# Performance work log

Measured on AMD Instinct MI355X. Metric: run time of the kernel, lower is better.

Reference implementation:

```python
import jax, jax.numpy as jnp
import numpy as np

EPS = 1e-6  # torch F.pairwise_distance default eps (added to the elementwise difference)
XI = 1.2


def _pdist(A, B):
    # dist[i, j] = || B[j] - A[i] + EPS ||_2  == || (B[j]+EPS) - A[i] ||_2
    Bp = B + EPS
    sq = (jnp.sum(Bp * Bp, axis=-1)[None, :]
          + jnp.sum(A * A, axis=-1)[:, None]
          - 2.0 * A @ Bp.T)
    return jnp.sqrt(jnp.maximum(sq, 0.0))


def _half_loss(D, M):
    # D: [B, B] distances, row i = anchor. M: [B, B] float same-label mask.
    same_max = jnp.max(D * M, axis=1)                      # max over same-label distances
    diff = D * (1.0 - M)                                   # zero at same-label slots
    diff_max = jnp.max(diff, axis=1)
    # replace same-label slots with diff_max so min picks the smallest diff-label distance
    diff_min = jnp.min(M * diff_max[:, None] + diff, axis=1)
    l = same_max - diff_min + XI
    return jnp.sum(jax.nn.relu(l))


def setup_inputs() -> dict:
    key = jax.random.key(0)
    k1, k2, k3 = jax.random.split(key, 3)
    B, d = 4096, 1024
    v_f = jax.random.normal(k1, (B, d), dtype=jnp.float32)
    i_f = jax.random.normal(k2, (B, d), dtype=jnp.float32)
    y = jax.random.randint(k3, (B,), 0, 64, dtype=jnp.int64)
    return {"v_f": v_f, "i_f": i_f, "y": y}


def reference(v_f, i_f, y):
    M = (y[:, None] == y[None, :]).astype(v_f.dtype)
    # loop 1: anchor i_f[i] vs all v_f  -> D1[i, j] = ||v_f[j] - i_f[i] + eps||
    loss_i = _half_loss(_pdist(i_f, v_f), M)
    # loop 2: anchor v_f[i] vs all i_f  -> D2[i, j] = ||i_f[j] - v_f[i] + eps||
    loss_v = _half_loss(_pdist(v_f, i_f), M)
    return loss_i + loss_v
```

## Files before the change

kernel.cpp:

```cpp
#include <hip/hip_runtime.h>
#include <hip/hip_bf16.h>


#define MDIM 4096
#define KDIM 1024
#define NT   16

typedef __attribute__((ext_vector_type(4))) float  f32x4;
typedef __attribute__((ext_vector_type(8))) short  bf16x8;

__device__ __forceinline__ void gload16(const void* g, void* l) {
  __builtin_amdgcn_global_load_lds(
      (const __attribute__((address_space(1))) void*)g,
      (__attribute__((address_space(3))) void*)l,
      16, 0, 0);
}

__device__ __forceinline__ unsigned short f2bf(float x) {
  unsigned int u = __float_as_uint(x);
  unsigned int r = (u + 0x7FFFu + ((u >> 16) & 1u)) >> 16;
  return (unsigned short)r;
}

#define BAR() do { asm volatile("" ::: "memory"); \
                   __builtin_amdgcn_s_barrier();  \
                   asm volatile("" ::: "memory"); } while (0)

__global__ __launch_bounds__(256) void prep_kernel(
    const float* __restrict__ vf, const float* __restrict__ iff,
    unsigned short* __restrict__ vb, unsigned short* __restrict__ ib,
    float* __restrict__ ni, float* __restrict__ nvp,
    int* __restrict__ same_sq, int* __restrict__ diff_sq,
    float* __restrict__ out) {
  const int wid = blockIdx.x * 4 + (threadIdx.x >> 6);
  const int lane = threadIdx.x & 63;
  const int mat = wid >> 12;
  const int row = wid & 4095;
  const float* X = mat ? iff : vf;
  unsigned short* Xb = mat ? ib : vb;

  const float4* xr4 = (const float4*)(X + (size_t)row * KDIM);
  ushort4* xb4 = (ushort4*)(Xb + (size_t)row * KDIM);

  float4 v = xr4[lane];
  ushort4 o;
  o.x = f2bf(v.x); o.y = f2bf(v.y); o.z = f2bf(v.z); o.w = f2bf(v.w);
  xb4[lane] = o;

  float s;
  if (mat) {
    s = v.x * v.x + v.y * v.y + v.z * v.z + v.w * v.w;
  } else {
    float ex = v.x + 1e-6f, ey = v.y + 1e-6f, ez = v.z + 1e-6f, ew = v.w + 1e-6f;
    s = ex * ex + ey * ey + ez * ez + ew * ew;
  }
  for (int off = 32; off; off >>= 1) s += __shfl_down(s, off);
  if (lane == 0) {
    if (mat) ni[row] = s; else nvp[row] = s;
  }

  const int gi = blockIdx.x * 256 + threadIdx.x;
  if (gi < 2 * MDIM) {
    same_sq[gi] = 0;
    diff_sq[gi] = 0x7F800000;
  }
  if (gi == 0) out[0] = 0.0f;
}

__global__ __launch_bounds__(512, 2) void tri_gemm(
    const unsigned short* __restrict__ vb, const unsigned short* __restrict__ ib,
    const float* __restrict__ ni, const float* __restrict__ nvp,
    const int* __restrict__ y,
    int* __restrict__ same_sq, int* __restrict__ diff_sq) {
  __shared__ unsigned short Abuf[2][256][64];
  __shared__ unsigned short Bbuf[2][256][64];
  __shared__ int   yrow[256], ycol[256];
  __shared__ float nAr[256], nBc[256];

  const unsigned short* Amat = ib;
  const unsigned short* Bmat = vb;

  const int row0 = blockIdx.y * 256;
  const int col0 = blockIdx.x * 256;

  const int t = threadIdx.x;
  const int w = t >> 6, lane = t & 63;
  const int lr = lane & 15, lg = lane >> 4;
  const int wr = w >> 2, wc = w & 3;

  auto stage = [&](const unsigned short* __restrict__ X, int tile0,
                   unsigned short (&buf)[256][64], int h, int k0s) {
#pragma unroll
    for (int r = 0; r < 2; ++r) {
      const int row = h * 128 + r * 64 + (t >> 3);
      const int chunk = t & 7;
      const unsigned short* src =
          X + (size_t)(tile0 + row) * KDIM + k0s + ((chunk ^ (row & 7)) << 3);
      gload16(src, &buf[h * 128 + r * 64 + (w << 3)][0]);
    }
  };
  auto ldA = [&](int c, int mh, int m, int ks) -> bf16x8 {
    const int row = wr * 128 + mh * 64 + m * 16 + lr;
    const int chunk = ((ks << 2) | lg) ^ (row & 7);
    return *(const bf16x8*)&Abuf[c][row][chunk << 3];
  };
  auto ldB = [&](int c, int nh, int n, int ks) -> bf16x8 {
    const int col = wc * 64 + nh * 32 + n * 16 + lr;
    const int chunk = ((ks << 2) | lg) ^ (col & 7);
    return *(const bf16x8*)&Bbuf[c][col][chunk << 3];
  };

  stage(Amat, row0, Abuf[0], 0, 0);
  stage(Amat, row0, Abuf[0], 1, 0);
  stage(Bmat, col0, Bbuf[0], 0, 0);
  stage(Bmat, col0, Bbuf[0], 1, 0);
  stage(Amat, row0, Abuf[1], 0, 64);
  if (t < 256) {
    yrow[t] = y[row0 + t];
    nAr[t] = ni[row0 + t];
  } else {
    const int c = t - 256;
    ycol[c] = y[col0 + c];
    nBc[c] = nvp[col0 + c];
  }
  asm volatile("s_waitcnt vmcnt(4) lgkmcnt(0)" ::: "memory");
  BAR();

  f32x4 acc[8][4] = {};
  bf16x8 aF[4][2], bF0[2][2], bF1[2][2];

#define DO_TILE(C, K1, K2)                                                     \
  do {                                                                         \
                              \
    _Pragma("unroll") for (int m = 0; m < 4; ++m) {                            \
      aF[m][0] = ldA(C, 0, m, 0);                                              \
      aF[m][1] = ldA(C, 0, m, 1);                                              \
    }                                                                          \
    _Pragma("unroll") for (int n = 0; n < 2; ++n) {                            \
      bF0[n][0] = ldB(C, 0, n, 0);                                             \
      bF0[n][1] = ldB(C, 0, n, 1);                                             \
    }                                                                          \
    stage(Amat, row0, Abuf[1 - (C)], 1, (K1));                                 \
    asm volatile("s_waitcnt lgkmcnt(8)" ::: "memory");                         \
    BAR();                                                                     \
    __builtin_amdgcn_s_setprio(1);                                             \
    _Pragma("unroll") for (int m = 0; m < 4; ++m)                              \
      _Pragma("unroll") for (int n = 0; n < 2; ++n) {                          \
        acc[m][n] = __builtin_amdgcn_mfma_f32_16x16x32_bf16(                   \
            aF[m][0], bF0[n][0], acc[m][n], 0, 0, 0);                          \
        acc[m][n] = __builtin_amdgcn_mfma_f32_16x16x32_bf16(                   \
            aF[m][1], bF0[n][1], acc[m][n], 0, 0, 0);                          \
      }                                                                        \
    __builtin_amdgcn_s_setprio(0);                                             \
    asm volatile("s_waitcnt vmcnt(4)" ::: "memory");                           \
    BAR();                                                                     \
                              \
    _Pragma("unroll") for (int n = 0; n < 2; ++n) {                            \
      bF1[n][0] = ldB(C, 1, n, 0);                                             \
      bF1[n][1] = ldB(C, 1, n, 1);                                             \
    }                                                                          \
    stage(Bmat, col0, Bbuf[1 - (C)], 0, (K1));                                 \
    BAR();                                                                     \
    __builtin_amdgcn_s_setprio(1);                                             \
    _Pragma("unroll") for (int m = 0; m < 4; ++m)                              \
      _Pragma("unroll") for (int n = 0; n < 2; ++n) {                          \
        acc[m][2 + n] = __builtin_amdgcn_mfma_f32_16x16x32_bf16(               \
            aF[m][0], bF1[n][0], acc[m][2 + n], 0, 0, 0);                      \
        acc[m][2 + n] = __builtin_amdgcn_mfma_f32_16x16x32_bf16(               \
            aF[m][1], bF1[n][1], acc[m][2 + n], 0, 0, 0);                      \
      }                                                                        \
    __builtin_amdgcn_s_setprio(0);                                             \
    BAR();                                                                     \
                              \
    _Pragma("unroll") for (int m = 0; m < 4; ++m) {                            \
      aF[m][0] = ldA(C, 1, m, 0);                                              \
      aF[m][1] = ldA(C, 1, m, 1);                                              \
    }                                                                          \
    stage(Bmat, col0, Bbuf[1 - (C)], 1, (K1));                                 \
    BAR();                                                                     \
    __builtin_amdgcn_s_setprio(1);                                             \
    _Pragma("unroll") for (int m = 0; m < 4; ++m)                              \
      _Pragma("unroll") for (int n = 0; n < 2; ++n) {                          \
        acc[4 + m][n] = __builtin_amdgcn_mfma_f32_16x16x32_bf16(               \
            aF[m][0], bF0[n][0], acc[4 + m][n], 0, 0, 0);                      \
        acc[4 + m][n] = __builtin_amdgcn_mfma_f32_16x16x32_bf16(               \
            aF[m][1], bF0[n][1], acc[4 + m][n], 0, 0, 0);                      \
      }                                                                        \
    __builtin_amdgcn_s_setprio(0);                                             \
    BAR();                                                                     \
                   \
    stage(Amat, row0, Abuf[C], 0, (K2));                                       \
    BAR();                                                                     \
    __builtin_amdgcn_s_setprio(1);                                             \
    _Pragma("unroll") for (int m = 0; m < 4; ++m)                              \
      _Pragma("unroll") for (int n = 0; n < 2; ++n) {                          \
        acc[4 + m][2 + n] = __builtin_amdgcn_mfma_f32_16x16x32_bf16(           \
            aF[m][0], bF1[n][0], acc[4 + m][2 + n], 0, 0, 0);                  \
        acc[4 + m][2 + n] = __builtin_amdgcn_mfma_f32_16x16x32_bf16(           \
            aF[m][1], bF1[n][1], acc[4 + m][2 + n], 0, 0, 0);                  \
      }                                                                        \
    __builtin_amdgcn_s_setprio(0);                                             \
    asm volatile("s_waitcnt vmcnt(4)" ::: "memory");                           \
    BAR();                                                                     \
  } while (0)

  for (int kt = 0; kt < NT; kt += 2) {
    const int ka = ((kt + 1) & (NT - 1)) * 64;
    const int kb = ((kt + 2) & (NT - 1)) * 64;
    const int kc = ((kt + 3) & (NT - 1)) * 64;
    DO_TILE(0, ka, kb);
    DO_TILE(1, kb, kc);
  }
#undef DO_TILE
  asm volatile("s_waitcnt vmcnt(0)" ::: "memory");

  const int rbase0 = row0;
  const int rbase1 = MDIM + col0;
  const float INF = __int_as_float(0x7F800000);

  float cs[4], cd[4];
#pragma unroll
  for (int N = 0; N < 4; ++N) { cs[N] = 0.0f; cd[N] = INF; }

#pragma unroll
  for (int M = 0; M < 8; ++M) {
#pragma unroll
    for (int r = 0; r < 4; ++r) {
      const int row_loc = wr * 128 + M * 16 + lg * 4 + r;
      const float na = nAr[row_loc];
      const int yl = yrow[row_loc];
      float smax = 0.0f;
      float dmin = INF;
#pragma unroll
      for (int N = 0; N < 4; ++N) {
        const int col_loc = wc * 64 + N * 16 + lr;
        const float sq = fmaxf(na + nBc[col_loc] - 2.0f * acc[M][N][r], 0.0f);
        if (ycol[col_loc] == yl) {
          smax = fmaxf(smax, sq);
          cs[N] = fmaxf(cs[N], sq);
        } else {
          dmin = fminf(dmin, sq);
          cd[N] = fminf(cd[N], sq);
        }
      }
#pragma unroll
      for (int off = 1; off < 16; off <<= 1) {
        smax = fmaxf(smax, __shfl_xor(smax, off));
        dmin = fminf(dmin, __shfl_xor(dmin, off));
      }
      if (lr == 0) {
        atomicMax(&same_sq[rbase0 + row_loc], __float_as_int(smax));
        atomicMin(&diff_sq[rbase0 + row_loc], __float_as_int(dmin));
      }
    }
  }
#pragma unroll
  for (int N = 0; N < 4; ++N) {
    float s = cs[N], d = cd[N];
    s = fmaxf(s, __shfl_xor(s, 16)); d = fminf(d, __shfl_xor(d, 16));
    s = fmaxf(s, __shfl_xor(s, 32)); d = fminf(d, __shfl_xor(d, 32));
    if (lane < 16) {
      const int col_loc = wc * 64 + N * 16 + lr;
      atomicMax(&same_sq[rbase1 + col_loc], __float_as_int(s));
      atomicMin(&diff_sq[rbase1 + col_loc], __float_as_int(d));
    }
  }
}

__global__ __launch_bounds__(256) void finalize_kernel(
    const int* __restrict__ same_sq, const int* __restrict__ diff_sq,
    float* __restrict__ out) {
  const int i = blockIdx.x * 256 + threadIdx.x;
  const float sm = sqrtf(__int_as_float(same_sq[i]));
  const float dm = sqrtf(__int_as_float(diff_sq[i]));
  float l = fmaxf(sm - dm + 1.2f, 0.0f);
  for (int off = 32; off; off >>= 1) l += __shfl_down(l, off);
  __shared__ float part[4];
  const int w = threadIdx.x >> 6, lane = threadIdx.x & 63;
  if (lane == 0) part[w] = l;
  __syncthreads();
  if (threadIdx.x == 0) atomicAdd(out, part[0] + part[1] + part[2] + part[3]);
}

extern "C" void kernel_launch(void* const* d_in, const int* in_sizes, int n_in,
                              void* d_out, int out_size, void* d_ws, size_t ws_size,
                              hipStream_t stream) {
  const float* vf = (const float*)d_in[0];
  const float* iff = (const float*)d_in[1];
  const int* y = (const int*)d_in[2];
  float* out = (float*)d_out;

  char* ws = (char*)d_ws;
  unsigned short* vb = (unsigned short*)ws;
  unsigned short* ib = (unsigned short*)(ws + (8u << 20));
  float* nv  = (float*)(ws + (16u << 20));
  float* ni  = nv + 4096;
  float* nvp = nv + 2 * 4096;
  int* same_sq = (int*)(nv + 4 * 4096);
  int* diff_sq = same_sq + 2 * 4096;

  prep_kernel<<<2048, 256, 0, stream>>>(vf, iff, vb, ib, ni, nvp,
                                        same_sq, diff_sq, out);
  tri_gemm<<<dim3(16, 16), 512, 0, stream>>>(vb, ib, ni, nvp, y,
                                             same_sq, diff_sq);
  finalize_kernel<<<32, 256, 0, stream>>>(same_sq, diff_sq, out);
}
```

Baseline: 55.91 us.

## Use 1024-thread blocks with 16 waves each owning a 64x64 sub-tile

Doubles the workgroup from 8 to 16 waves over the same 256x256 output tile. Each wave now accumulates a 64x64 region instead of 128x64, which halves accumulator registers. Each thread issues one global-to-LDS load per stage instead of two, and the prologue waitcnt and per-tile waitcnt are adjusted to match. This aims to add latency hiding through more resident waves, at the cost of more barrier participants and lower MFMA work per LDS fragment load.

New measurement: 65.04 us. +16.3%, slower.

```diff
diff --git a/kernel.cpp b/kernel.cpp
--- a/kernel.cpp
+++ b/kernel.cpp
@@ -67,7 +67,7 @@
   if (gi == 0) out[0] = 0.0f;
 }
 
-__global__ __launch_bounds__(512, 2) void tri_gemm(
+__global__ __launch_bounds__(1024, 4) void tri_gemm(
     const unsigned short* __restrict__ vb, const unsigned short* __restrict__ ib,
     const float* __restrict__ ni, const float* __restrict__ nvp,
     const int* __restrict__ y,
@@ -90,17 +90,14 @@
 
   auto stage = [&](const unsigned short* __restrict__ X, int tile0,
                    unsigned short (&buf)[256][64], int h, int k0s) {
-#pragma unroll
-    for (int r = 0; r < 2; ++r) {
-      const int row = h * 128 + r * 64 + (t >> 3);
-      const int chunk = t & 7;
-      const unsigned short* src =
-          X + (size_t)(tile0 + row) * KDIM + k0s + ((chunk ^ (row & 7)) << 3);
-      gload16(src, &buf[h * 128 + r * 64 + (w << 3)][0]);
-    }
+    const int row = h * 128 + (t >> 3);
+    const int chunk = t & 7;
+    const unsigned short* src =
+        X + (size_t)(tile0 + row) * KDIM + k0s + ((chunk ^ (row & 7)) << 3);
+    gload16(src, &buf[h * 128 + (w << 3)][0]);
   };
   auto ldA = [&](int c, int mh, int m, int ks) -> bf16x8 {
-    const int row = wr * 128 + mh * 64 + m * 16 + lr;
+    const int row = wr * 64 + mh * 32 + m * 16 + lr;
     const int chunk = ((ks << 2) | lg) ^ (row & 7);
     return *(const bf16x8*)&Abuf[c][row][chunk << 3];
   };
@@ -115,92 +112,80 @@
   stage(Bmat, col0, Bbuf[0], 0, 0);
   stage(Bmat, col0, Bbuf[0], 1, 0);
   stage(Amat, row0, Abuf[1], 0, 64);
+  stage(Amat, row0, Abuf[1], 1, 64);
   if (t < 256) {
     yrow[t] = y[row0 + t];
     nAr[t] = ni[row0 + t];
-  } else {
+  } else if (t < 512) {
     const int c = t - 256;
     ycol[c] = y[col0 + c];
     nBc[c] = nvp[col0 + c];
   }
-  asm volatile("s_waitcnt vmcnt(4) lgkmcnt(0)" ::: "memory");
+  asm volatile("s_waitcnt vmcnt(2) lgkmcnt(0)" ::: "memory");
   BAR();
 
-  f32x4 acc[8][4] = {};
-  bf16x8 aF[4][2], bF0[2][2], bF1[2][2];
+  f32x4 acc[4][4] = {};
+  bf16x8 aF[2][2], bF0[2][2], bF1[2][2];
 
 #define DO_TILE(C, K1, K2)                                                     \
   do {                                                                         \
-                              \
-    _Pragma("unroll") for (int m = 0; m < 4; ++m) {                            \
-      aF[m][0] = ldA(C, 0, m, 0);                                              \
-      aF[m][1] = ldA(C, 0, m, 1);                                              \
-    }                                                                          \
-    _Pragma("unroll") for (int n = 0; n < 2; ++n) {                            \
-      bF0[n][0] = ldB(C, 0, n, 0);                                             \
-      bF0[n][1] = ldB(C, 0, n, 1);                                             \
-    }                                                                          \
-    stage(Amat, row0, Abuf[1 - (C)], 1, (K1));                                 \
-    asm volatile("s_waitcnt lgkmcnt(8)" ::: "memory");                         \
-    BAR();                                                                     \
-    __builtin_amdgcn_s_setprio(1);                                             \
-    _Pragma("unroll") for (int m = 0; m < 4; ++m)                              \
-      _Pragma("unroll") for (int n = 0; n < 2; ++n) {                          \
-        acc[m][n] = __builtin_amdgcn_mfma_f32_16x16x32_bf16(                   \
-            aF[m][0], bF0[n][0], acc[m][n], 0, 0, 0);                          \
-        acc[m][n] = __builtin_amdgcn_mfma_f32_16x16x32_bf16(                   \
-            aF[m][1], bF0[n][1], acc[m][n], 0, 0, 0);                          \
-      }                                                                        \
-    __builtin_amdgcn_s_setprio(0);                                             \
-    asm volatile("s_waitcnt vmcnt(4)" ::: "memory");                           \
-    BAR();                                                                     \
-                              \
-    _Pragma("unroll") for (int n = 0; n < 2; ++n) {                            \
-      bF1[n][0] = ldB(C, 1, n, 0);                                             \
-      bF1[n][1] = ldB(C, 1, n, 1);                                             \
-    }                                                                          \
+                      \
+    _Pragma("unroll") for (int m = 0; m < 2; ++m)                              \
+      _Pragma("unroll") for (int ks = 0; ks < 2; ++ks)                         \
+        aF[m][ks] = ldA(C, 0, m, ks);                                          \
+    _Pragma("unroll") for (int n = 0; n < 2; ++n)                              \
+      _Pragma("unroll") for (int ks = 0; ks < 2; ++ks)                         \
+        bF0[n][ks] = ldB(C, 0, n, ks);                                         \
     stage(Bmat, col0, Bbuf[1 - (C)], 0, (K1));                                 \
     BAR();                                                                     \
     __builtin_amdgcn_s_setprio(1);                                             \
-    _Pragma("unroll") for (int m = 0; m < 4; ++m)                              \
-      _Pragma("unroll") for (int n = 0; n < 2; ++n) {                          \
-        acc[m][2 + n] = __builtin_amdgcn_mfma_f32_16x16x32_bf16(               \
-            aF[m][0], bF1[n][0], acc[m][2 + n], 0, 0, 0);                      \
-        acc[m][2 + n] = __builtin_amdgcn_mfma_f32_16x16x32_bf16(               \
-            aF[m][1], bF1[n][1], acc[m][2 + n], 0, 0, 0);                      \
-      }                                                                        \
-    __builtin_amdgcn_s_setprio(0);                                             \
-    BAR();                                                                     \
-                              \
-    _Pragma("unroll") for (int m = 0; m < 4; ++m) {                            \
-      aF[m][0] = ldA(C, 1, m, 0);                                              \
-      aF[m][1] = ldA(C, 1, m, 1);                                              \
-    }                                                                          \
+    _Pragma("unroll") for (int m = 0; m < 2; ++m)                              \
+      _Pragma("unroll") for (int n = 0; n < 2; ++n)                            \
+        _Pragma("unroll") for (int ks = 0; ks < 2; ++ks)                       \
+          acc[m][n] = __builtin_amdgcn_mfma_f32_16x16x32_bf16(                 \
+              aF[m][ks], bF0[n][ks], acc[m][n], 0, 0, 0);                      \
+    __builtin_amdgcn_s_setprio(0);                                             \
+    BAR();                                                                     \
+                                 \
+    _Pragma("unroll") for (int n = 0; n < 2; ++n)                              \
+      _Pragma("unroll") for (int ks = 0; ks < 2; ++ks)                         \
+        bF1[n][ks] = ldB(C, 1, n, ks);                                         \
     stage(Bmat, col0, Bbuf[1 - (C)], 1, (K1));                                 \
     BAR();                                                                     \
     __builtin_amdgcn_s_setprio(1);                                             \
-    _Pragma("unroll") for (int m = 0; m < 4; ++m)                              \
-      _Pragma("unroll") for (int n = 0; n < 2; ++n) {                          \
-        acc[4 + m][n] = __builtin_amdgcn_mfma_f32_16x16x32_bf16(               \
-            aF[m][0], bF0[n][0], acc[4 + m][n], 0, 0, 0);                      \
-        acc[4 + m][n] = __builtin_amdgcn_mfma_f32_16x16x32_bf16(               \
-            aF[m][1], bF0[n][1], acc[4 + m][n], 0, 0, 0);                      \
-      }                                                                        \
-    __builtin_amdgcn_s_setprio(0);                                             \
-    BAR();                                                                     \
-                   \
+    _Pragma("unroll") for (int m = 0; m < 2; ++m)                              \
+      _Pragma("unroll") for (int n = 0; n < 2; ++n)                            \
+        _Pragma("unroll") for (int ks = 0; ks < 2; ++ks)                       \
+          acc[m][2 + n] = __builtin_amdgcn_mfma_f32_16x16x32_bf16(             \
+              aF[m][ks], bF1[n][ks], acc[m][2 + n], 0, 0, 0);                  \
+    __builtin_amdgcn_s_setprio(0);                                             \
+    BAR();                                                                     \
+                                             \
+    _Pragma("unroll") for (int m = 0; m < 2; ++m)                              \
+      _Pragma("unroll") for (int ks = 0; ks < 2; ++ks)                         \
+        aF[m][ks] = ldA(C, 1, m, ks);                                          \
+    BAR();                                                                     \
+    __builtin_amdgcn_s_setprio(1);                                             \
+    _Pragma("unroll") for (int m = 0; m < 2; ++m)                              \
+      _Pragma("unroll") for (int n = 0; n < 2; ++n)                            \
+        _Pragma("unroll") for (int ks = 0; ks < 2; ++ks)                       \
+          acc[2 + m][n] = __builtin_amdgcn_mfma_f32_16x16x32_bf16(             \
+              aF[m][ks], bF0[n][ks], acc[2 + m][n], 0, 0, 0);                  \
+    __builtin_amdgcn_s_setprio(0);                                             \
+    BAR();                                                                     \
+        \
+               \
     stage(Amat, row0, Abuf[C], 0, (K2));                                       \
-    BAR();                                                                     \
-    __builtin_amdgcn_s_setprio(1);                                             \
-    _Pragma("unroll") for (int m = 0; m < 4; ++m)                              \
-      _Pragma("unroll") for (int n = 0; n < 2; ++n) {                          \
-        acc[4 + m][2 + n] = __builtin_amdgcn_mfma_f32_16x16x32_bf16(           \
-            aF[m][0], bF1[n][0], acc[4 + m][2 + n], 0, 0, 0);                  \
-        acc[4 + m][2 + n] = __builtin_amdgcn_mfma_f32_16x16x32_bf16(           \
-            aF[m][1], bF1[n][1], acc[4 + m][2 + n], 0, 0, 0);                  \
-      }                                                                        \
-    __builtin_amdgcn_s_setprio(0);                                             \
-    asm volatile("s_waitcnt vmcnt(4)" ::: "memory");                           \
+    stage(Amat, row0, Abuf[C], 1, (K2));                                       \
+    BAR();                                                                     \
+    __builtin_amdgcn_s_setprio(1);                                             \
+    _Pragma("unroll") for (int m = 0; m < 2; ++m)                              \
+      _Pragma("unroll") for (int n = 0; n < 2; ++n)                            \
+        _Pragma("unroll") for (int ks = 0; ks < 2; ++ks)                       \
+          acc[2 + m][2 + n] = __builtin_amdgcn_mfma_f32_16x16x32_bf16(         \
+              aF[m][ks], bF1[n][ks], acc[2 + m][2 + n], 0, 0, 0);              \
+    __builtin_amdgcn_s_setprio(0);                                             \
+    asm volatile("s_waitcnt vmcnt(2)" ::: "memory");                           \
     BAR();                                                                     \
   } while (0)
 
@@ -223,10 +208,10 @@
   for (int N = 0; N < 4; ++N) { cs[N] = 0.0f; cd[N] = INF; }
 
 #pragma unroll
-  for (int M = 0; M < 8; ++M) {
+  for (int M = 0; M < 4; ++M) {
 #pragma unroll
     for (int r = 0; r < 4; ++r) {
-      const int row_loc = wr * 128 + M * 16 + lg * 4 + r;
+      const int row_loc = wr * 64 + M * 16 + lg * 4 + r;
       const float na = nAr[row_loc];
       const int yl = yrow[row_loc];
       float smax = 0.0f;
@@ -301,7 +286,7 @@
 
   prep_kernel<<<2048, 256, 0, stream>>>(vf, iff, vb, ib, ni, nvp,
                                         same_sq, diff_sq, out);
-  tri_gemm<<<dim3(16, 16), 512, 0, stream>>>(vb, ib, ni, nvp, y,
-                                             same_sq, diff_sq);
+  tri_gemm<<<dim3(16, 16), 1024, 0, stream>>>(vb, ib, ni, nvp, y,
+                                              same_sq, diff_sq);
   finalize_kernel<<<32, 256, 0, stream>>>(same_sq, diff_sq, out);
 }
```
